# Performance work log

Measured on AMD Instinct MI355X. Metric: run time of the kernel, lower is better.

Reference implementation:

```python
import jax, jax.numpy as jnp
import numpy as np

RANK, A1, A2, B1, B2 = 64, 64, 64, 64, 64
N_TOKENS = 8192


def _xavier_uniform(key, shape, fan_in, fan_out, dtype=jnp.float32):
    bound = float(np.sqrt(6.0 / (fan_in + fan_out)))
    return jax.random.uniform(key, shape, dtype, -bound, bound)


def setup_inputs() -> dict:
    key = jax.random.key(0)
    kx, ka, kb, kbias = jax.random.split(key, 4)
    x = jax.random.normal(kx, (N_TOKENS, A1 * B1), dtype=jnp.float32)
    # torch xavier on a 3D tensor (rank, d1, d2): fan_in = d1*d2, fan_out = rank*d2
    a = _xavier_uniform(ka, (RANK, A1, A2), A1 * A2, RANK * A2)
    b = _xavier_uniform(kb, (RANK, B1, B2), B1 * B2, RANK * B2)
    bias = jax.random.normal(kbias, (A2 * B2,), dtype=jnp.float32)
    return {"x": x, "a": a, "b": b, "bias": bias}


def reference(x, a, b, bias):
    r, a1, a2 = a.shape
    _, b1, b2 = b.shape
    # w = sum_r kron(a_r, b_r):  w[i*b1+k, j*b2+l] = sum_r a[r,i,j] * b[r,k,l]
    w = jnp.einsum('rij,rkl->ikjl', a, b).reshape(a1 * b1, a2 * b2)
    out = x @ w  # (N, a2*b2)
    return out + bias[None, :]
```

## Files before the change

### kernel.cpp

```cpp
#include <hip/hip_runtime.h>
#include <hip/hip_bf16.h>


#define M_DIM 8192
#define N_DIM 4096
#define K_DIM 4096
#define KT_COUNT 128

typedef __attribute__((ext_vector_type(8))) short short8;
typedef __attribute__((ext_vector_type(4))) float floatx4;

typedef __attribute__((address_space(1))) void gvoid_t;
typedef __attribute__((address_space(3))) void lvoid_t;

static __device__ __forceinline__ void gl_lds16(const void* g, const void* l) {
  __builtin_amdgcn_global_load_lds((gvoid_t*)(unsigned long long)g,
                                   (lvoid_t*)(unsigned int)(unsigned long long)l,
                                   16, 0, 0);
}

static __device__ __forceinline__ unsigned short f2bf(float f) {
  unsigned int u = __builtin_bit_cast(unsigned int, f);
  u = (u + 0x7fffu + ((u >> 16) & 1u)) >> 16;
  return (unsigned short)u;
}

__global__ __launch_bounds__(256) void prep_kernel(
    const float* __restrict__ x, const float* __restrict__ a,
    const float* __restrict__ b, unsigned short* __restrict__ Xp,
    unsigned short* __restrict__ Wp) {
  __shared__ float lds[128 * 33];
  const int bid = blockIdx.x;
  const int t = threadIdx.x;

  if (bid < 2048) {
    const int rg = bid & 255;
    const int i = rg >> 2;
    const int j0 = (rg & 3) * 16;
    const int k0 = (bid >> 8) * 8;

    {
      const int r = t >> 2, jq = t & 3;
      float4 v = ((const float4*)(a + (size_t)r * 4096 + i * 64 + j0))[jq];
      ((float4*)lds)[r * 4 + jq] = v;
    }
    __syncthreads();

    const int l = t & 63;
    const int jj = t >> 6;
    float acc[4][8];
#pragma unroll
    for (int jp = 0; jp < 4; ++jp)
#pragma unroll
      for (int kb = 0; kb < 8; ++kb) acc[jp][kb] = 0.f;

    const float* bb = b + k0 * 64 + l;
#pragma unroll 4
    for (int r = 0; r < 64; ++r) {
      float4 aj = ((const float4*)lds)[r * 4 + jj];
      float bv[8];
#pragma unroll
      for (int kb = 0; kb < 8; ++kb) bv[kb] = bb[(size_t)r * 4096 + kb * 64];
      const float av[4] = {aj.x, aj.y, aj.z, aj.w};
#pragma unroll
      for (int jp = 0; jp < 4; ++jp)
#pragma unroll
        for (int kb = 0; kb < 8; ++kb)
          acc[jp][kb] = fmaf(av[jp], bv[kb], acc[jp][kb]);
    }

    const int kt = (i * 64 + k0) >> 5;
    const int c = (k0 & 31) >> 3;
#pragma unroll
    for (int jp = 0; jp < 4; ++jp) {
      const int j = j0 + jj * 4 + jp;
      const int n = j * 64 + l;
      const int blob = (n >> 7) * KT_COUNT + kt;
      const int pos = c * 128 + (n & 127);
      short8 o;
#pragma unroll
      for (int kb = 0; kb < 8; ++kb) o[kb] = (short)f2bf(acc[jp][kb]);
      *(short8*)(Wp + (size_t)blob * 4096 + pos * 8) = o;
    }
  } else {
    const int pid = bid - 2048;
    const int kt = pid & 127;
    const int M0 = pid >> 7;

    {
      const int row = t >> 1;
      const int half = t & 1;
      const float* src = x + (size_t)(M0 * 128 + row) * K_DIM + kt * 32 + half * 16;
      float v[16];
#pragma unroll
      for (int w = 0; w < 4; ++w) {
        float4 vv = ((const float4*)src)[w];
        v[w * 4 + 0] = vv.x; v[w * 4 + 1] = vv.y;
        v[w * 4 + 2] = vv.z; v[w * 4 + 3] = vv.w;
      }
#pragma unroll
      for (int e = 0; e < 16; ++e) lds[row * 33 + half * 16 + e] = v[e];
    }
    __syncthreads();

    unsigned short* dst = Xp + (size_t)(M0 * KT_COUNT + kt) * 4096;
#pragma unroll
    for (int q = 0; q < 2; ++q) {
      const int p = q * 256 + t;
      const int c = p >> 7, mm = p & 127;
      short8 o;
#pragma unroll
      for (int j = 0; j < 8; ++j) o[j] = (short)f2bf(lds[mm * 33 + c * 8 + j]);
      *(short8*)(dst + p * 8) = o;
    }
  }
}

#define BAR() asm volatile("s_barrier" ::: "memory")
#define WAIT_VM(N) asm volatile("s_waitcnt vmcnt(" #N ")" ::: "memory")
#define WAIT_LGKM0() asm volatile("s_waitcnt lgkmcnt(0)" ::: "memory")

__global__ __launch_bounds__(512, 2) void gemm_kernel(
    const unsigned short* __restrict__ Xp, const unsigned short* __restrict__ Wp,
    const float* __restrict__ bias, float* __restrict__ out) {
  __shared__ short8 As[4][2][512];
  __shared__ short8 Bs[4][2][512];

  const int bid = blockIdx.x;
  const int xcd = bid & 7;
  const int pos = bid >> 3;
  const int N0 = xcd * 2 + (pos & 1);
  const int M0 = pos >> 1;

  const int t = threadIdx.x;
  const int wave = t >> 6, lane = t & 63;
  const int l16 = lane & 15, quad = lane >> 4;
  const int wm = wave & 1;
  const int wn = wave >> 1;

  floatx4 acc[8][4];
#pragma unroll
  for (int mt = 0; mt < 8; ++mt)
#pragma unroll
    for (int nt = 0; nt < 4; ++nt) acc[mt][nt] = (floatx4){0.f, 0.f, 0.f, 0.f};

  const unsigned short* gA0 = Xp + (size_t)(M0 * 2 + 0) * KT_COUNT * 4096 + (size_t)t * 8;
  const unsigned short* gA1 = Xp + (size_t)(M0 * 2 + 1) * KT_COUNT * 4096 + (size_t)t * 8;
  const unsigned short* gB0 = Wp + (size_t)(N0 * 2 + 0) * KT_COUNT * 4096 + (size_t)t * 8;
  const unsigned short* gB1 = Wp + (size_t)(N0 * 2 + 1) * KT_COUNT * 4096 + (size_t)t * 8;

  gl_lds16(gA0, &As[0][0][t]);
  gl_lds16(gA1, &As[0][1][t]);
  gl_lds16(gB0, &Bs[0][0][t]);
  gl_lds16(gB1, &Bs[0][1][t]);
  gl_lds16(gA0 + 4096, &As[1][0][t]);
  gl_lds16(gA1 + 4096, &As[1][1][t]);
  gl_lds16(gB0 + 4096, &Bs[1][0][t]);
  gl_lds16(gB1 + 4096, &Bs[1][1][t]);
  WAIT_VM(4);
  BAR();

  const int ra = quad * 128 + l16;
  const int rb = quad * 128 + (wn & 1) * 64 + l16;
  const int bh = wn >> 1;

#pragma unroll 2
  for (int kt = 0; kt < KT_COUNT; ++kt) {
    const int tb = kt & 3;
    const int db = (kt + 2) & 3;
    const size_t soff =
        (size_t)((kt + 2 < KT_COUNT) ? kt + 2 : KT_COUNT - 1) * 4096;

    short8 bf[4], af[4];

#pragma unroll
    for (int nt = 0; nt < 4; ++nt) bf[nt] = Bs[tb][bh][rb + nt * 16];
#pragma unroll
    for (int m = 0; m < 4; ++m) af[m] = As[tb][wm][ra + m * 16];
    gl_lds16(gA0 + soff, &As[db][0][t]);
    gl_lds16(gA1 + soff, &As[db][1][t]);
    BAR();
    WAIT_LGKM0();
    __builtin_amdgcn_sched_barrier(0);
    __builtin_amdgcn_s_setprio(1);
#pragma unroll
    for (int m = 0; m < 4; ++m)
#pragma unroll
      for (int nt = 0; nt < 4; ++nt)
        acc[m][nt] = __builtin_amdgcn_mfma_f32_16x16x32_bf16(
            af[m], bf[nt], acc[m][nt], 0, 0, 0);
    __builtin_amdgcn_s_setprio(0);
    __builtin_amdgcn_sched_barrier(0);
    BAR();

#pragma unroll
    for (int m = 0; m < 4; ++m) af[m] = As[tb][wm][ra + (4 + m) * 16];
    gl_lds16(gB0 + soff, &Bs[db][0][t]);
    gl_lds16(gB1 + soff, &Bs[db][1][t]);
    WAIT_VM(4);
    BAR();
    WAIT_LGKM0();
    __builtin_amdgcn_sched_barrier(0);
    __builtin_amdgcn_s_setprio(1);
#pragma unroll
    for (int m = 0; m < 4; ++m)
#pragma unroll
      for (int nt = 0; nt < 4; ++nt)
        acc[4 + m][nt] = __builtin_amdgcn_mfma_f32_16x16x32_bf16(
            af[m], bf[nt], acc[4 + m][nt], 0, 0, 0);
    __builtin_amdgcn_s_setprio(0);
    __builtin_amdgcn_sched_barrier(0);
    BAR();
  }

  const int col_base = N0 * 256 + wn * 64;
  const int row_base = M0 * 256 + wm * 128;
#pragma unroll
  for (int nt = 0; nt < 4; ++nt) {
    const int col = col_base + nt * 16 + l16;
    const float bv = bias[col];
#pragma unroll
    for (int mt = 0; mt < 8; ++mt) {
      floatx4 v = acc[mt][nt];
#pragma unroll
      for (int r4 = 0; r4 < 4; ++r4) {
        const int row = row_base + mt * 16 + quad * 4 + r4;
        out[(size_t)row * N_DIM + col] = v[r4] + bv;
      }
    }
  }
}

extern "C" void kernel_launch(void* const* d_in, const int* in_sizes, int n_in,
                              void* d_out, int out_size, void* d_ws, size_t ws_size,
                              hipStream_t stream) {
  const float* x = (const float*)d_in[0];
  const float* a = (const float*)d_in[1];
  const float* b = (const float*)d_in[2];
  const float* bias = (const float*)d_in[3];
  float* out = (float*)d_out;

  unsigned short* Xp = (unsigned short*)d_ws;
  unsigned short* Wp = Xp + (size_t)M_DIM * K_DIM;

  prep_kernel<<<2048 + 8192, 256, 0, stream>>>(x, a, b, Xp, Wp);
  gemm_kernel<<<512, 512, 0, stream>>>(Xp, Wp, bias, out);
}
```

Baseline: 480.5 us.

## Simplify X packing layout and deepen GEMM prefetch pipeline to three stages

The X conversion to bf16 now streams contiguous rows directly into a permuted blob layout without an LDS transpose. The GEMM compensates by remapping each thread's global source offset for A so that the LDS contents stay the same. The GEMM also prefetches three k-tiles ahead instead of two, with the vmcnt waits adjusted to match. The W prep blocks now run at 512 threads with half of them idle. This trades some occupancy in W prep for cheaper X packing and more latency hiding in the main loop.

```diff
diff --git a/kernel.cpp b/kernel.cpp
--- a/kernel.cpp
+++ b/kernel.cpp
@@ -6,6 +6,7 @@
 #define N_DIM 4096
 #define K_DIM 4096
 #define KT_COUNT 128
+#define NPACK 512
 
 typedef __attribute__((ext_vector_type(8))) short short8;
 typedef __attribute__((ext_vector_type(4))) float floatx4;
@@ -25,93 +26,85 @@
   return (unsigned short)u;
 }
 
-__global__ __launch_bounds__(256) void prep_kernel(
+__global__ __launch_bounds__(512) void prep_kernel(
     const float* __restrict__ x, const float* __restrict__ a,
     const float* __restrict__ b, unsigned short* __restrict__ Xp,
     unsigned short* __restrict__ Wp) {
-  __shared__ float lds[128 * 33];
+  __shared__ float lds_a[1024];
   const int bid = blockIdx.x;
   const int t = threadIdx.x;
 
-  if (bid < 2048) {
-    const int rg = bid & 255;
+  if (bid < NPACK) {
+    const int M0 = bid >> 3;
+    const int mm0 = (bid & 7) * 16;
+    const int kt = t >> 2, c = t & 3;
+    const float* src = x + (size_t)(M0 * 128 + mm0) * K_DIM + t * 8;
+    unsigned short* dst =
+        Xp + (size_t)(M0 * KT_COUNT + kt) * 4096 + (mm0 * 4 + c) * 8;
+#pragma unroll 4
+    for (int r = 0; r < 16; ++r) {
+      float4 v0 = ((const float4*)src)[0];
+      float4 v1 = ((const float4*)src)[1];
+      short8 o;
+      o[0] = (short)f2bf(v0.x); o[1] = (short)f2bf(v0.y);
+      o[2] = (short)f2bf(v0.z); o[3] = (short)f2bf(v0.w);
+      o[4] = (short)f2bf(v1.x); o[5] = (short)f2bf(v1.y);
+      o[6] = (short)f2bf(v1.z); o[7] = (short)f2bf(v1.w);
+      *(short8*)dst = o;
+      src += K_DIM;
+      dst += 32;
+    }
+  } else {
+    const int bw = bid - NPACK;
+    const int rg = bw & 255;
     const int i = rg >> 2;
     const int j0 = (rg & 3) * 16;
-    const int k0 = (bid >> 8) * 8;
-
-    {
+    const int k0 = (bw >> 8) * 8;
+
+    if (t < 256) {
       const int r = t >> 2, jq = t & 3;
       float4 v = ((const float4*)(a + (size_t)r * 4096 + i * 64 + j0))[jq];
-      ((float4*)lds)[r * 4 + jq] = v;
+      ((float4*)lds_a)[r * 4 + jq] = v;
     }
     __syncthreads();
 
-    const int l = t & 63;
-    const int jj = t >> 6;
-    float acc[4][8];
-#pragma unroll
-    for (int jp = 0; jp < 4; ++jp)
-#pragma unroll
-      for (int kb = 0; kb < 8; ++kb) acc[jp][kb] = 0.f;
-
-    const float* bb = b + k0 * 64 + l;
+    if (t < 256) {
+      const int l = t & 63;
+      const int jj = t >> 6;
+      float acc[4][8];
+#pragma unroll
+      for (int jp = 0; jp < 4; ++jp)
+#pragma unroll
+        for (int kb = 0; kb < 8; ++kb) acc[jp][kb] = 0.f;
+
+      const float* bb = b + k0 * 64 + l;
 #pragma unroll 4
-    for (int r = 0; r < 64; ++r) {
-      float4 aj = ((const float4*)lds)[r * 4 + jj];
-      float bv[8];
-#pragma unroll
-      for (int kb = 0; kb < 8; ++kb) bv[kb] = bb[(size_t)r * 4096 + kb * 64];
-      const float av[4] = {aj.x, aj.y, aj.z, aj.w};
-#pragma unroll
-      for (int jp = 0; jp < 4; ++jp)
-#pragma unroll
-        for (int kb = 0; kb < 8; ++kb)
-          acc[jp][kb] = fmaf(av[jp], bv[kb], acc[jp][kb]);
-    }
-
-    const int kt = (i * 64 + k0) >> 5;
-    const int c = (k0 & 31) >> 3;
-#pragma unroll
-    for (int jp = 0; jp < 4; ++jp) {
-      const int j = j0 + jj * 4 + jp;
-      const int n = j * 64 + l;
-      const int blob = (n >> 7) * KT_COUNT + kt;
-      const int pos = c * 128 + (n & 127);
-      short8 o;
-#pragma unroll
-      for (int kb = 0; kb < 8; ++kb) o[kb] = (short)f2bf(acc[jp][kb]);
-      *(short8*)(Wp + (size_t)blob * 4096 + pos * 8) = o;
-    }
-  } else {
-    const int pid = bid - 2048;
-    const int kt = pid & 127;
-    const int M0 = pid >> 7;
-
-    {
-      const int row = t >> 1;
-      const int half = t & 1;
-      const float* src = x + (size_t)(M0 * 128 + row) * K_DIM + kt * 32 + half * 16;
-      float v[16];
-#pragma unroll
-      for (int w = 0; w < 4; ++w) {
-        float4 vv = ((const float4*)src)[w];
-        v[w * 4 + 0] = vv.x; v[w * 4 + 1] = vv.y;
-        v[w * 4 + 2] = vv.z; v[w * 4 + 3] = vv.w;
+      for (int r = 0; r < 64; ++r) {
+        float4 aj = ((const float4*)lds_a)[r * 4 + jj];
+        float bv[8];
+#pragma unroll
+        for (int kb = 0; kb < 8; ++kb) bv[kb] = bb[(size_t)r * 4096 + kb * 64];
+        const float av[4] = {aj.x, aj.y, aj.z, aj.w};
+#pragma unroll
+        for (int jp = 0; jp < 4; ++jp)
+#pragma unroll
+          for (int kb = 0; kb < 8; ++kb)
+            acc[jp][kb] = fmaf(av[jp], bv[kb], acc[jp][kb]);
       }
-#pragma unroll
-      for (int e = 0; e < 16; ++e) lds[row * 33 + half * 16 + e] = v[e];
-    }
-    __syncthreads();
-
-    unsigned short* dst = Xp + (size_t)(M0 * KT_COUNT + kt) * 4096;
-#pragma unroll
-    for (int q = 0; q < 2; ++q) {
-      const int p = q * 256 + t;
-      const int c = p >> 7, mm = p & 127;
-      short8 o;
-#pragma unroll
-      for (int j = 0; j < 8; ++j) o[j] = (short)f2bf(lds[mm * 33 + c * 8 + j]);
-      *(short8*)(dst + p * 8) = o;
+
+      const int kt = (i * 64 + k0) >> 5;
+      const int c = (k0 & 31) >> 3;
+#pragma unroll
+      for (int jp = 0; jp < 4; ++jp) {
+        const int j = j0 + jj * 4 + jp;
+        const int n = j * 64 + l;
+        const int blob = (n >> 7) * KT_COUNT + kt;
+        const int pos = c * 128 + (n & 127);
+        short8 o;
+#pragma unroll
+        for (int kb = 0; kb < 8; ++kb) o[kb] = (short)f2bf(acc[jp][kb]);
+        *(short8*)(Wp + (size_t)blob * 4096 + pos * 8) = o;
+      }
     }
   }
 }
@@ -144,20 +137,20 @@
 #pragma unroll
     for (int nt = 0; nt < 4; ++nt) acc[mt][nt] = (floatx4){0.f, 0.f, 0.f, 0.f};
 
-  const unsigned short* gA0 = Xp + (size_t)(M0 * 2 + 0) * KT_COUNT * 4096 + (size_t)t * 8;
-  const unsigned short* gA1 = Xp + (size_t)(M0 * 2 + 1) * KT_COUNT * 4096 + (size_t)t * 8;
+  const int pt = ((t & 127) << 2) | (t >> 7);
+  const unsigned short* gA0 = Xp + (size_t)(M0 * 2 + 0) * KT_COUNT * 4096 + (size_t)pt * 8;
+  const unsigned short* gA1 = Xp + (size_t)(M0 * 2 + 1) * KT_COUNT * 4096 + (size_t)pt * 8;
   const unsigned short* gB0 = Wp + (size_t)(N0 * 2 + 0) * KT_COUNT * 4096 + (size_t)t * 8;
   const unsigned short* gB1 = Wp + (size_t)(N0 * 2 + 1) * KT_COUNT * 4096 + (size_t)t * 8;
 
-  gl_lds16(gA0, &As[0][0][t]);
-  gl_lds16(gA1, &As[0][1][t]);
-  gl_lds16(gB0, &Bs[0][0][t]);
-  gl_lds16(gB1, &Bs[0][1][t]);
-  gl_lds16(gA0 + 4096, &As[1][0][t]);
-  gl_lds16(gA1 + 4096, &As[1][1][t]);
-  gl_lds16(gB0 + 4096, &Bs[1][0][t]);
-  gl_lds16(gB1 + 4096, &Bs[1][1][t]);
-  WAIT_VM(4);
+#pragma unroll
+  for (int s = 0; s < 3; ++s) {
+    gl_lds16(gA0 + (size_t)s * 4096, &As[s][0][t]);
+    gl_lds16(gA1 + (size_t)s * 4096, &As[s][1][t]);
+    gl_lds16(gB0 + (size_t)s * 4096, &Bs[s][0][t]);
+    gl_lds16(gB1 + (size_t)s * 4096, &Bs[s][1][t]);
+  }
+  WAIT_VM(8);
   BAR();
 
   const int ra = quad * 128 + l16;
@@ -167,9 +160,9 @@
 #pragma unroll 2
   for (int kt = 0; kt < KT_COUNT; ++kt) {
     const int tb = kt & 3;
-    const int db = (kt + 2) & 3;
+    const int db = (kt + 3) & 3;
     const size_t soff =
-        (size_t)((kt + 2 < KT_COUNT) ? kt + 2 : KT_COUNT - 1) * 4096;
+        (size_t)((kt + 3 < KT_COUNT) ? kt + 3 : KT_COUNT - 1) * 4096;
 
     short8 bf[4], af[4];
 
@@ -197,7 +190,7 @@
     for (int m = 0; m < 4; ++m) af[m] = As[tb][wm][ra + (4 + m) * 16];
     gl_lds16(gB0 + soff, &Bs[db][0][t]);
     gl_lds16(gB1 + soff, &Bs[db][1][t]);
-    WAIT_VM(4);
+    WAIT_VM(8);
     BAR();
     WAIT_LGKM0();
     __builtin_amdgcn_sched_barrier(0);
@@ -243,6 +236,6 @@
   unsigned short* Xp = (unsigned short*)d_ws;
   unsigned short* Wp = Xp + (size_t)M_DIM * K_DIM;
 
-  prep_kernel<<<2048 + 8192, 256, 0, stream>>>(x, a, b, Xp, Wp);
+  prep_kernel<<<NPACK + 2048, 512, 0, stream>>>(x, a, b, Xp, Wp);
   gemm_kernel<<<512, 512, 0, stream>>>(Xp, Wp, bias, out);
 }
```

After: 487.1 us. No clear change (+1.4%).

## Split prep into W-build and X-pack kernels with LDS-staged b tiles

Applied to the files above, without the earlier changes.

Splits the fused prep kernel into two launches. build_w_kernel now stages b rows into double-buffered LDS via global_load_lds, overlapping the next group's load with FMA work instead of issuing strided global loads per thread. pack_x_kernel converts x to bf16 before the LDS transpose and uses an XOR-swizzled short8 layout, with larger blocks covering more of K. This cuts LDS traffic and bank conflicts in exchange for an extra kernel launch.

```diff
diff --git a/kernel.cpp b/kernel.cpp
--- a/kernel.cpp
+++ b/kernel.cpp
@@ -25,100 +25,132 @@
   return (unsigned short)u;
 }
 
-__global__ __launch_bounds__(256) void prep_kernel(
-    const float* __restrict__ x, const float* __restrict__ a,
-    const float* __restrict__ b, unsigned short* __restrict__ Xp,
-    unsigned short* __restrict__ Wp) {
-  __shared__ float lds[128 * 33];
-  const int bid = blockIdx.x;
-  const int t = threadIdx.x;
-
-  if (bid < 2048) {
-    const int rg = bid & 255;
-    const int i = rg >> 2;
-    const int j0 = (rg & 3) * 16;
-    const int k0 = (bid >> 8) * 8;
-
-    {
-      const int r = t >> 2, jq = t & 3;
-      float4 v = ((const float4*)(a + (size_t)r * 4096 + i * 64 + j0))[jq];
-      ((float4*)lds)[r * 4 + jq] = v;
-    }
-    __syncthreads();
-
-    const int l = t & 63;
-    const int jj = t >> 6;
-    float acc[4][8];
-#pragma unroll
-    for (int jp = 0; jp < 4; ++jp)
-#pragma unroll
-      for (int kb = 0; kb < 8; ++kb) acc[jp][kb] = 0.f;
-
-    const float* bb = b + k0 * 64 + l;
-#pragma unroll 4
-    for (int r = 0; r < 64; ++r) {
-      float4 aj = ((const float4*)lds)[r * 4 + jj];
-      float bv[8];
-#pragma unroll
-      for (int kb = 0; kb < 8; ++kb) bv[kb] = bb[(size_t)r * 4096 + kb * 64];
-      const float av[4] = {aj.x, aj.y, aj.z, aj.w};
-#pragma unroll
-      for (int jp = 0; jp < 4; ++jp)
-#pragma unroll
-        for (int kb = 0; kb < 8; ++kb)
-          acc[jp][kb] = fmaf(av[jp], bv[kb], acc[jp][kb]);
-    }
-
-    const int kt = (i * 64 + k0) >> 5;
-    const int c = (k0 & 31) >> 3;
-#pragma unroll
-    for (int jp = 0; jp < 4; ++jp) {
-      const int j = j0 + jj * 4 + jp;
-      const int n = j * 64 + l;
-      const int blob = (n >> 7) * KT_COUNT + kt;
-      const int pos = c * 128 + (n & 127);
-      short8 o;
-#pragma unroll
-      for (int kb = 0; kb < 8; ++kb) o[kb] = (short)f2bf(acc[jp][kb]);
-      *(short8*)(Wp + (size_t)blob * 4096 + pos * 8) = o;
-    }
-  } else {
-    const int pid = bid - 2048;
-    const int kt = pid & 127;
-    const int M0 = pid >> 7;
-
-    {
-      const int row = t >> 1;
-      const int half = t & 1;
-      const float* src = x + (size_t)(M0 * 128 + row) * K_DIM + kt * 32 + half * 16;
-      float v[16];
-#pragma unroll
-      for (int w = 0; w < 4; ++w) {
-        float4 vv = ((const float4*)src)[w];
-        v[w * 4 + 0] = vv.x; v[w * 4 + 1] = vv.y;
-        v[w * 4 + 2] = vv.z; v[w * 4 + 3] = vv.w;
-      }
-#pragma unroll
-      for (int e = 0; e < 16; ++e) lds[row * 33 + half * 16 + e] = v[e];
-    }
-    __syncthreads();
-
-    unsigned short* dst = Xp + (size_t)(M0 * KT_COUNT + kt) * 4096;
-#pragma unroll
-    for (int q = 0; q < 2; ++q) {
-      const int p = q * 256 + t;
-      const int c = p >> 7, mm = p & 127;
-      short8 o;
-#pragma unroll
-      for (int j = 0; j < 8; ++j) o[j] = (short)f2bf(lds[mm * 33 + c * 8 + j]);
-      *(short8*)(dst + p * 8) = o;
-    }
-  }
-}
-
 #define BAR() asm volatile("s_barrier" ::: "memory")
 #define WAIT_VM(N) asm volatile("s_waitcnt vmcnt(" #N ")" ::: "memory")
 #define WAIT_LGKM0() asm volatile("s_waitcnt lgkmcnt(0)" ::: "memory")
+
+__global__ __launch_bounds__(256) void build_w_kernel(
+    const float* __restrict__ a, const float* __restrict__ b,
+    unsigned short* __restrict__ Wp) {
+  __shared__ float lds_a[1024];
+  __shared__ float lds_b[2][4096];
+  const int bid = blockIdx.x;
+  const int t = threadIdx.x;
+  const int rg = bid & 255;
+  const int i = rg >> 2;
+  const int j0 = (rg & 3) * 16;
+  const int k0 = (bid >> 8) * 8;
+
+  {
+    const int r = t >> 2, jq = t & 3;
+    float4 v = ((const float4*)(a + (size_t)r * 4096 + i * 64 + j0))[jq];
+    ((float4*)lds_a)[r * 4 + jq] = v;
+  }
+
+  const float* bsrc = b + k0 * 64;
+
+#pragma unroll
+  for (int p = 0; p < 4; ++p) {
+    const int idx = p * 256 + t;
+    gl_lds16(bsrc + (size_t)(idx >> 7) * 4096 + (idx & 127) * 4,
+             &((float4*)lds_b[0])[idx]);
+  }
+  WAIT_VM(0);
+  __syncthreads();
+
+  const int l = t & 63;
+  const int jj = t >> 6;
+  float acc[4][8];
+#pragma unroll
+  for (int jp = 0; jp < 4; ++jp)
+#pragma unroll
+    for (int kb = 0; kb < 8; ++kb) acc[jp][kb] = 0.f;
+
+  for (int g = 0; g < 8; ++g) {
+    const int cur = g & 1;
+    if (g < 7) {
+      const float* nb = bsrc + (size_t)(g + 1) * 8 * 4096;
+#pragma unroll
+      for (int p = 0; p < 4; ++p) {
+        const int idx = p * 256 + t;
+        gl_lds16(nb + (size_t)(idx >> 7) * 4096 + (idx & 127) * 4,
+                 &((float4*)lds_b[cur ^ 1])[idx]);
+      }
+    }
+#pragma unroll
+    for (int rr = 0; rr < 8; ++rr) {
+      float4 aj = ((const float4*)lds_a)[(g * 8 + rr) * 4 + jj];
+      float bv[8];
+#pragma unroll
+      for (int kb = 0; kb < 8; ++kb) bv[kb] = lds_b[cur][rr * 512 + kb * 64 + l];
+      const float av[4] = {aj.x, aj.y, aj.z, aj.w};
+#pragma unroll
+      for (int jp = 0; jp < 4; ++jp)
+#pragma unroll
+        for (int kb = 0; kb < 8; ++kb)
+          acc[jp][kb] = fmaf(av[jp], bv[kb], acc[jp][kb]);
+    }
+    WAIT_VM(0);
+    __syncthreads();
+  }
+
+  const int kt = (i * 64 + k0) >> 5;
+  const int cw = (k0 & 31) >> 3;
+#pragma unroll
+  for (int jp = 0; jp < 4; ++jp) {
+    const int j = j0 + jj * 4 + jp;
+    const int n = j * 64 + l;
+    const int blob = (n >> 7) * KT_COUNT + kt;
+    const int pos = cw * 128 + (n & 127);
+    short8 o;
+#pragma unroll
+    for (int kb = 0; kb < 8; ++kb) o[kb] = (short)f2bf(acc[jp][kb]);
+    *(short8*)(Wp + (size_t)blob * 4096 + pos * 8) = o;
+  }
+}
+
+__global__ __launch_bounds__(512) void pack_x_kernel(
+    const float* __restrict__ x, unsigned short* __restrict__ Xp) {
+  __shared__ short8 smem[2048];
+  const int pid = blockIdx.x;
+  const int M0 = pid >> 5;
+  const int h = (pid >> 4) & 1;
+  const int kg = pid & 15;
+  const int t = threadIdx.x;
+
+  {
+    const int rsub = t >> 5;
+    const int col8 = t & 31;
+#pragma unroll
+    for (int p = 0; p < 4; ++p) {
+      const int rr = p * 16 + rsub;
+      const float* src =
+          x + (size_t)(M0 * 128 + h * 64 + rr) * K_DIM + kg * 256 + col8 * 8;
+      float4 v0 = ((const float4*)src)[0];
+      float4 v1 = ((const float4*)src)[1];
+      short8 o;
+      o[0] = (short)f2bf(v0.x); o[1] = (short)f2bf(v0.y);
+      o[2] = (short)f2bf(v0.z); o[3] = (short)f2bf(v0.w);
+      o[4] = (short)f2bf(v1.x); o[5] = (short)f2bf(v1.y);
+      o[6] = (short)f2bf(v1.z); o[7] = (short)f2bf(v1.w);
+      smem[rr * 32 + (col8 ^ (rr & 31))] = o;
+    }
+  }
+  __syncthreads();
+
+  const int ml = t & 63;
+  const int c = (t >> 6) & 3;
+  const int qh = t >> 8;
+#pragma unroll
+  for (int q = 0; q < 4; ++q) {
+    const int qq = q * 2 + qh;
+    const int cc = qq * 4 + c;
+    short8 v = smem[ml * 32 + (cc ^ (ml & 31))];
+    unsigned short* dst = Xp + (size_t)(M0 * KT_COUNT + kg * 8 + qq) * 4096 +
+                          (size_t)(c * 128 + h * 64 + ml) * 8;
+    *(short8*)dst = v;
+  }
+}
 
 __global__ __launch_bounds__(512, 2) void gemm_kernel(
     const unsigned short* __restrict__ Xp, const unsigned short* __restrict__ Wp,
@@ -243,6 +275,7 @@
   unsigned short* Xp = (unsigned short*)d_ws;
   unsigned short* Wp = Xp + (size_t)M_DIM * K_DIM;
 
-  prep_kernel<<<2048 + 8192, 256, 0, stream>>>(x, a, b, Xp, Wp);
+  build_w_kernel<<<2048, 256, 0, stream>>>(a, b, Wp);
+  pack_x_kernel<<<2048, 512, 0, stream>>>(x, Xp);
   gemm_kernel<<<512, 512, 0, stream>>>(Xp, Wp, bias, out);
 }
```

Measured after the change: 474.2 us. About the same (-1.3%).
